# Kernel optimization log

Measured on AMD Instinct MI355X. Metric: run time of the kernel, lower is better.

Reference implementation:

```python
import jax, jax.numpy as jnp
import numpy as np

B, H, K, D = 4096, 512, 32, 20


def setup_inputs() -> dict:
    key = jax.random.key(0)
    k1, k2 = jax.random.split(key)
    hidden = jax.random.normal(k1, (B, H), dtype=jnp.float32)
    # cluster: soft assignment probabilities (rows sum to 1), like a softmax output
    c = jax.random.uniform(k2, (B, K), dtype=jnp.float32)
    cluster = c / jnp.sum(c, axis=-1, keepdims=True)
    return {"hidden": hidden, "cluster": cluster, "d": D}


def reference(hidden, cluster, d):
    # softHidden[b,h,k] = hidden[b,h] * cluster[b,k]
    soft_hidden = hidden[:, :, None] * cluster[:, None, :]          # [B,H,K]
    class_sums = jnp.sum(soft_hidden, axis=0)                        # [H,K] (code calls these "class_means" but they are sums)
    within = jnp.sum((soft_hidden - class_sums[None]) ** 2, axis=0)  # [H,K]
    # round() has zero gradient in torch; mirror that with stop_gradient
    counts = jax.lax.stop_gradient(jnp.round(jnp.sum(cluster, axis=0)))  # [K]

    m = class_sums.T   # [K,H]
    w = within.T       # [K,H]

    # all class pairs i<j (the nested Python loops, vectorized)
    i, j = jnp.triu_indices(K, k=1)   # each [P], P = K*(K-1)/2
    mi, mj = m[i], m[j]                               # [P,H]
    gm = (mi + mj) / 2.0
    between = (mi - gm) ** 2 * counts[i][:, None] + (mj - gm) ** 2 * counts[j][:, None]
    pair_within = w[i] + w[j]                         # [P,H]
    pair_count = counts[i] + counts[j]                # [P]

    d2 = pair_count - 2.0
    d2 = jnp.where(d2 == 0.0, d2 + 1e-5, d2)
    x = between / (between + pair_within)
    x = jnp.clip(x, 1e-37, 1.0 - 1e-5)
    # regularized incomplete beta I_x(d1/2, d2/2) with d1 = 1
    xbetainc = jax.scipy.special.betainc(0.5, (d2 / 2.0)[:, None], x)  # [P,H]

    top_k, _ = jax.lax.top_k(xbetainc, d)             # [P,d]
    per_pair = jnp.sum(jnp.log(top_k), axis=-1)       # [P]
    return -jnp.sum(per_pair)
```

## Files before the change

kernel.cpp:

```cpp
#include <hip/hip_runtime.h>
#include <math.h>

#define BB 4096
#define HH 512
#define KK 32
#define PAIRS ((KK * (KK - 1)) / 2)

constexpr int TH  = 16;
constexpr int NBB = 16;
constexpr int BC  = BB / NBB;
constexpr int SUB = 64;
constexpr int RP  = TH + 1;


__global__ __launch_bounds__(256) void stage1_kernel(
    const float* __restrict__ hidden, const float* __restrict__ cluster,
    float* __restrict__ part_m, float* __restrict__ part_s,
    float* __restrict__ pcol, float* __restrict__ ctl)
{
    __shared__ float hid_s[SUB * TH];
    __shared__ float clu_s[SUB * KK];
    __shared__ float red  [8 * KK * RP];
    __shared__ float cred [8 * KK];

    const int t  = threadIdx.x;
    const int ty = t >> 5;
    const int tx = t & 31;
    const int h0 = blockIdx.x * TH;
    const int c  = blockIdx.y;
    const int bchunk = c * BC;

    if (blockIdx.x == 0 && c == 0 && t == 0) {
        ctl[0] = 0.0f;
        ((unsigned*)ctl)[1] = 0u;
    }

    float acc_m[TH], acc_s[TH];
#pragma unroll
    for (int i = 0; i < TH; ++i) { acc_m[i] = 0.f; acc_s[i] = 0.f; }
    float csum = 0.f;

    const float4* hid4 = (const float4*)hidden;
    const float4* clu4 = (const float4*)cluster;

    for (int sub = 0; sub < BC; sub += SUB) {
        const int b0 = bchunk + sub;
        {
            int r = t >> 2, q = t & 3;
            ((float4*)hid_s)[t] =
                hid4[(size_t)(b0 + r) * (HH / 4) + (h0 >> 2) + q];
        }
#pragma unroll
        for (int e = 0; e < 2; ++e) {
            int u = t + e * 256;
            int r = u >> 3, q = u & 7;
            ((float4*)clu_s)[u] = clu4[(size_t)(b0 + r) * (KK / 4) + q];
        }
        __syncthreads();

#pragma unroll
        for (int s = 0; s < SUB / 8; ++s) {
            int r = s * 8 + ty;
            float cc = clu_s[r * KK + tx];
            float c2 = cc * cc;
            csum += cc;
#pragma unroll
            for (int hh = 0; hh < TH; ++hh) {
                float hv = hid_s[r * TH + hh];
                acc_m[hh] = fmaf(hv,      cc, acc_m[hh]);
                acc_s[hh] = fmaf(hv * hv, c2, acc_s[hh]);
            }
        }
        __syncthreads();
    }

    cred[ty * KK + tx] = csum;
    __syncthreads();
    if (blockIdx.x == 0 && t < KK) {
        float v = 0.f;
#pragma unroll
        for (int g = 0; g < 8; ++g) v += cred[g * KK + t];
        pcol[c * KK + t] = v;
    }

#pragma unroll
    for (int hh = 0; hh < TH; ++hh)
        red[ty * (KK * RP) + tx * RP + hh] = acc_m[hh];
    __syncthreads();
    for (int u = t; u < KK * TH; u += 256) {
        int k = u >> 4, hh = u & 15;
        float v = 0.f;
#pragma unroll
        for (int g = 0; g < 8; ++g) v += red[g * (KK * RP) + k * RP + hh];
        part_m[((size_t)c * KK + k) * HH + h0 + hh] = v;
    }
    __syncthreads();
#pragma unroll
    for (int hh = 0; hh < TH; ++hh)
        red[ty * (KK * RP) + tx * RP + hh] = acc_s[hh];
    __syncthreads();
    for (int u = t; u < KK * TH; u += 256) {
        int k = u >> 4, hh = u & 15;
        float v = 0.f;
#pragma unroll
        for (int g = 0; g < 8; ++g) v += red[g * (KK * RP) + k * RP + hh];
        part_s[((size_t)c * KK + k) * HH + h0 + hh] = v;
    }
}

__device__ __forceinline__ float frcp(float x) {
#if __has_builtin(__builtin_amdgcn_rcpf)
    return __builtin_amdgcn_rcpf(x);
#else
    return 1.0f / x;
#endif
}
__device__ __forceinline__ float guardf(float t) {
    return (fabsf(t) < 1e-30f) ? 1e-30f : t;
}

__device__ float betacf_fast(float a, float b, float x)
{
    const float EPS = 1e-5f;
    float qab = a + b, qap = a + 1.0f, qam = a - 1.0f;
    float c = 1.0f;
    float d = frcp(guardf(1.0f - qab * x * frcp(qap)));
    float h = d;
    for (int m = 1; m <= 100; ++m) {
        float fm = (float)m, m2 = 2.0f * fm;
        float aa = fm * (b - fm) * x * frcp((qam + m2) * (a + m2));
        d = frcp(guardf(fmaf(aa, d, 1.0f)));
        c = guardf(fmaf(aa, frcp(c), 1.0f));
        h *= d * c;
        float aa2 = -(a + fm) * (qab + fm) * x * frcp((a + m2) * (qap + m2));
        d = frcp(guardf(fmaf(aa2, d, 1.0f)));
        c = guardf(fmaf(aa2, frcp(c), 1.0f));
        float del = d * c;
        h *= del;
        if (__all(fabsf(del - 1.0f) < EPS)) break;
    }
    return h;
}

__global__ __launch_bounds__(256) void stage2_kernel(
    const float* __restrict__ part_m, const float* __restrict__ part_s,
    const float* __restrict__ pcol, float* __restrict__ ctl,
    const int* __restrict__ dptr, float* __restrict__ out)
{
    __shared__ float xs[HH];

    const int t = threadIdx.x;
    const int w = t >> 6, lane = t & 63;
    const int p = blockIdx.x;

    int i = 0, rem = p;
    while (true) { int row = KK - 1 - i; if (rem < row) break; rem -= row; ++i; }
    const int j = i + 1 + rem;

    float ci = 0.f, cj = 0.f;
#pragma unroll
    for (int cc = 0; cc < NBB; ++cc) {
        ci += pcol[cc * KK + i];
        cj += pcol[cc * KK + j];
    }
    ci = roundf(ci); cj = roundf(cj);
    const float pc = ci + cj;
    float d2 = pc - 2.0f;
    if (d2 == 0.0f) d2 = 1e-5f;
    const float a = 0.5f;
    const float b = 0.5f * d2;

#pragma unroll
    for (int q = 0; q < 2; ++q) {
        int h = w * 128 + q * 64 + lane;
        float mi = 0.f, mj = 0.f, si = 0.f, sj = 0.f;
#pragma unroll
        for (int cc = 0; cc < NBB; ++cc) {
            size_t base = (size_t)cc * KK * HH;
            mi += part_m[base + (size_t)i * HH + h];
            mj += part_m[base + (size_t)j * HH + h];
            si += part_s[base + (size_t)i * HH + h];
            sj += part_s[base + (size_t)j * HH + h];
        }
        float wi = fmaf((float)(BB - 2) * mi, mi, si);
        float wj = fmaf((float)(BB - 2) * mj, mj, sj);
        float dm = 0.5f * (mi - mj);
        float between = dm * dm * pc;
        float denom = between + wi + wj;
        float x = between / denom;
        if (!(x >= 1e-37f)) x = 1e-37f;
        x = fminf(x, 1.0f - 1e-5f);
        xs[h] = x;
    }
    __syncthreads();
    if (w != 0) return;

    float lv[8];
#pragma unroll
    for (int q = 0; q < 8; ++q) lv[q] = xs[q * 64 + lane];

    const int d = *dptr;
    const float lg = lgammaf(a + b) - lgammaf(b) - 0.57236494f;
    const float xsplit = (a + 1.0f) / (a + b + 2.0f);

    float myx = 0.004f;
    float lm = lv[0];
#pragma unroll
    for (int q = 1; q < 8; ++q) lm = fmaxf(lm, lv[q]);

    for (int r = 0; r < d; ++r) {
        float gm = lm;
#pragma unroll
        for (int off = 1; off < 64; off <<= 1)
            gm = fmaxf(gm, __shfl_xor(gm, off));
        unsigned long long msk = __ballot(lm == gm);
        int winner = __ffsll((unsigned long long)msk) - 1;
        if (lane == r) myx = gm;
        if (lane == winner) {
            bool done = false;
#pragma unroll
            for (int q = 0; q < 8; ++q)
                if (!done && lv[q] == gm) { lv[q] = -1.0f; done = true; }
            lm = lv[0];
#pragma unroll
            for (int q = 1; q < 8; ++q) lm = fmaxf(lm, lv[q]);
        }
    }

    float x   = myx;
    float omx = 1.0f - x;
    bool  brA = x < xsplit;
    float al  = brA ? a : b;
    float be  = brA ? b : a;
    float xx  = brA ? x : omx;
    float cf  = betacf_fast(al, be, xx);
    float lbt = lg + 0.5f * logf(x) + b * logf(omx);
    float L;
    if (brA) {
        L = lbt + logf(2.0f * fmaxf(cf, 1e-30f));
    } else {
        float tt = expf(lbt) * cf / b;
        tt = fminf(tt, 0.99999988f);
        L = log1pf(-tt);
    }

    float val = (lane < d) ? L : 0.0f;
#pragma unroll
    for (int off = 1; off < 64; off <<= 1) val += __shfl_xor(val, off);

    if (lane == 0) {
        atomicAdd(&ctl[0], -val);
        __threadfence();
        unsigned old = atomicAdd((unsigned*)ctl + 1, 1u);
        if (old == PAIRS - 1) {
            out[0] = atomicAdd(&ctl[0], 0.0f);
        }
    }
}

extern "C" void kernel_launch(void* const* d_in, const int* in_sizes, int n_in,
                              void* d_out, int out_size, void* d_ws, size_t ws_size,
                              hipStream_t stream)
{
    const float* hidden  = (const float*)d_in[0];
    const float* cluster = (const float*)d_in[1];
    const int*   dptr    = (const int*)d_in[2];

    float* part_m = (float*)d_ws;
    float* part_s = part_m + (size_t)NBB * KK * HH;
    float* pcol   = part_s + (size_t)NBB * KK * HH;
    float* ctl    = pcol + NBB * KK;

    dim3 g1(HH / TH, NBB);
    stage1_kernel<<<g1, 256, 0, stream>>>(hidden, cluster,
                                          part_m, part_s, pcol, ctl);
    stage2_kernel<<<PAIRS, 256, 0, stream>>>(part_m, part_s, pcol, ctl,
                                             dptr, (float*)d_out);
}
```

Measured before the change: 95.35 us.

## Replace continued-fraction betainc with closed-form series for integer degrees of freedom

For integer d2 (the Student-t style case with a=1/2), stage2 now evaluates the regularized incomplete beta with a finite closed-form series. The series uses compile-time coefficient tables plus asin for odd cases, and it replaces the iterative Lentz continued fraction and lgamma calls. Stage1 also precomputes squared hidden values into shared memory and reads hidden tiles as float4, which cuts per-element multiplies and LDS instructions. The series loop length grows with d2 (around 128 here), so the cost is a table-driven loop with global constant loads, and the old path remains as a fallback for non-integer values.

```diff
diff --git a/kernel.cpp b/kernel.cpp
--- a/kernel.cpp
+++ b/kernel.cpp
@@ -12,16 +12,33 @@
 constexpr int SUB = 64;
 constexpr int RP  = TH + 1;
 
+struct TabE {
+    float v[2048];
+    constexpr TabE() : v{} {
+        double c = 1.0; v[0] = 1.0f;
+        for (int j = 1; j < 2048; ++j) { c *= (2.0*j - 1.0) / (2.0*j); v[j] = (float)c; }
+    }
+};
+struct TabO {
+    float v[2048];
+    constexpr TabO() : v{} {
+        double c = 1.0; v[0] = 1.0f;
+        for (int j = 1; j < 2048; ++j) { c *= (2.0*j) / (2.0*j + 1.0); v[j] = (float)c; }
+    }
+};
+__device__ constexpr TabE tab_e{};
+__device__ constexpr TabO tab_o{};
 
 __global__ __launch_bounds__(256) void stage1_kernel(
     const float* __restrict__ hidden, const float* __restrict__ cluster,
     float* __restrict__ part_m, float* __restrict__ part_s,
     float* __restrict__ pcol, float* __restrict__ ctl)
 {
-    __shared__ float hid_s[SUB * TH];
-    __shared__ float clu_s[SUB * KK];
-    __shared__ float red  [8 * KK * RP];
-    __shared__ float cred [8 * KK];
+    __shared__ float hid_s [SUB * TH];
+    __shared__ float hid2_s[SUB * TH];
+    __shared__ float clu_s [SUB * KK];
+    __shared__ float red   [8 * KK * RP];
+    __shared__ float cred  [8 * KK];
 
     const int t  = threadIdx.x;
     const int ty = t >> 5;
@@ -47,8 +64,10 @@
         const int b0 = bchunk + sub;
         {
             int r = t >> 2, q = t & 3;
-            ((float4*)hid_s)[t] =
-                hid4[(size_t)(b0 + r) * (HH / 4) + (h0 >> 2) + q];
+            float4 v = hid4[(size_t)(b0 + r) * (HH / 4) + (h0 >> 2) + q];
+            ((float4*)hid_s)[t] = v;
+            float4 v2; v2.x = v.x*v.x; v2.y = v.y*v.y; v2.z = v.z*v.z; v2.w = v.w*v.w;
+            ((float4*)hid2_s)[t] = v2;
         }
 #pragma unroll
         for (int e = 0; e < 2; ++e) {
@@ -58,18 +77,32 @@
         }
         __syncthreads();
 
+        const float4* h4 = (const float4*)hid_s;
+        const float4* g4 = (const float4*)hid2_s;
 #pragma unroll
         for (int s = 0; s < SUB / 8; ++s) {
             int r = s * 8 + ty;
             float cc = clu_s[r * KK + tx];
             float c2 = cc * cc;
             csum += cc;
-#pragma unroll
-            for (int hh = 0; hh < TH; ++hh) {
-                float hv = hid_s[r * TH + hh];
-                acc_m[hh] = fmaf(hv,      cc, acc_m[hh]);
-                acc_s[hh] = fmaf(hv * hv, c2, acc_s[hh]);
-            }
+            float4 a0 = h4[r*4+0], a1 = h4[r*4+1], a2 = h4[r*4+2], a3 = h4[r*4+3];
+            float4 b0 = g4[r*4+0], b1 = g4[r*4+1], b2 = g4[r*4+2], b3 = g4[r*4+3];
+            acc_m[0]  = fmaf(a0.x, cc, acc_m[0]);  acc_m[1]  = fmaf(a0.y, cc, acc_m[1]);
+            acc_m[2]  = fmaf(a0.z, cc, acc_m[2]);  acc_m[3]  = fmaf(a0.w, cc, acc_m[3]);
+            acc_m[4]  = fmaf(a1.x, cc, acc_m[4]);  acc_m[5]  = fmaf(a1.y, cc, acc_m[5]);
+            acc_m[6]  = fmaf(a1.z, cc, acc_m[6]);  acc_m[7]  = fmaf(a1.w, cc, acc_m[7]);
+            acc_m[8]  = fmaf(a2.x, cc, acc_m[8]);  acc_m[9]  = fmaf(a2.y, cc, acc_m[9]);
+            acc_m[10] = fmaf(a2.z, cc, acc_m[10]); acc_m[11] = fmaf(a2.w, cc, acc_m[11]);
+            acc_m[12] = fmaf(a3.x, cc, acc_m[12]); acc_m[13] = fmaf(a3.y, cc, acc_m[13]);
+            acc_m[14] = fmaf(a3.z, cc, acc_m[14]); acc_m[15] = fmaf(a3.w, cc, acc_m[15]);
+            acc_s[0]  = fmaf(b0.x, c2, acc_s[0]);  acc_s[1]  = fmaf(b0.y, c2, acc_s[1]);
+            acc_s[2]  = fmaf(b0.z, c2, acc_s[2]);  acc_s[3]  = fmaf(b0.w, c2, acc_s[3]);
+            acc_s[4]  = fmaf(b1.x, c2, acc_s[4]);  acc_s[5]  = fmaf(b1.y, c2, acc_s[5]);
+            acc_s[6]  = fmaf(b1.z, c2, acc_s[6]);  acc_s[7]  = fmaf(b1.w, c2, acc_s[7]);
+            acc_s[8]  = fmaf(b2.x, c2, acc_s[8]);  acc_s[9]  = fmaf(b2.y, c2, acc_s[9]);
+            acc_s[10] = fmaf(b2.z, c2, acc_s[10]); acc_s[11] = fmaf(b2.w, c2, acc_s[11]);
+            acc_s[12] = fmaf(b3.x, c2, acc_s[12]); acc_s[13] = fmaf(b3.y, c2, acc_s[13]);
+            acc_s[14] = fmaf(b3.z, c2, acc_s[14]); acc_s[15] = fmaf(b3.w, c2, acc_s[15]);
         }
         __syncthreads();
     }
@@ -167,7 +200,6 @@
     const float pc = ci + cj;
     float d2 = pc - 2.0f;
     if (d2 == 0.0f) d2 = 1e-5f;
-    const float a = 0.5f;
     const float b = 0.5f * d2;
 
 #pragma unroll
@@ -200,9 +232,6 @@
     for (int q = 0; q < 8; ++q) lv[q] = xs[q * 64 + lane];
 
     const int d = *dptr;
-    const float lg = lgammaf(a + b) - lgammaf(b) - 0.57236494f;
-    const float xsplit = (a + 1.0f) / (a + b + 2.0f);
-
     float myx = 0.004f;
     float lm = lv[0];
 #pragma unroll
@@ -227,21 +256,60 @@
         }
     }
 
-    float x   = myx;
-    float omx = 1.0f - x;
-    bool  brA = x < xsplit;
-    float al  = brA ? a : b;
-    float be  = brA ? b : a;
-    float xx  = brA ? x : omx;
-    float cf  = betacf_fast(al, be, xx);
-    float lbt = lg + 0.5f * logf(x) + b * logf(omx);
+    float x  = myx;
+    float u  = 1.0f - x;
+    float sx = sqrtf(x);
+    int nu = (int)(d2 + 0.5f);
     float L;
-    if (brA) {
-        L = lbt + logf(2.0f * fmaxf(cf, 1e-30f));
+    if (nu >= 1 && nu <= 4094 && fabsf(d2 - (float)nu) < 1e-3f) {
+        float u2 = u * u;
+        if (nu & 1) {
+            int terms = (nu - 1) >> 1;
+            float S = 0.f;
+            if (terms > 0) {
+                float S0 = 0.f, S1 = 0.f, p0 = 1.f, p1 = u;
+                int jj = 0;
+                for (; jj + 1 < terms; jj += 2) {
+                    S0 = fmaf(tab_o.v[jj],     p0, S0);
+                    S1 = fmaf(tab_o.v[jj + 1], p1, S1);
+                    p0 *= u2; p1 *= u2;
+                }
+                if (jj < terms) S0 = fmaf(tab_o.v[jj], p0, S0);
+                S = S0 + S1;
+            }
+            float theta = asinf(fminf(sx, 1.0f));
+            float A = 0.636619772367581343f * (theta + sx * sqrtf(u) * S);
+            L = logf(fminf(A, 1.0f));
+        } else {
+            int terms = nu >> 1;
+            float S0 = 0.f, S1 = 0.f, p0 = 1.f, p1 = u;
+            int jj = 0;
+            for (; jj + 1 < terms; jj += 2) {
+                S0 = fmaf(tab_e.v[jj],     p0, S0);
+                S1 = fmaf(tab_e.v[jj + 1], p1, S1);
+                p0 *= u2; p1 *= u2;
+            }
+            if (jj < terms) S0 = fmaf(tab_e.v[jj], p0, S0);
+            float A = sx * (S0 + S1);
+            L = logf(fminf(A, 1.0f));
+        }
     } else {
-        float tt = expf(lbt) * cf / b;
-        tt = fminf(tt, 0.99999988f);
-        L = log1pf(-tt);
+        const float a = 0.5f;
+        const float lg = lgammaf(a + b) - lgammaf(b) - 0.57236494f;
+        const float xsplit = (a + 1.0f) / (a + b + 2.0f);
+        bool  brA = x < xsplit;
+        float al  = brA ? a : b;
+        float be  = brA ? b : a;
+        float xx  = brA ? x : u;
+        float cf  = betacf_fast(al, be, xx);
+        float lbt = lg + 0.5f * logf(x) + b * logf(u);
+        if (brA) {
+            L = lbt + logf(2.0f * fmaxf(cf, 1e-30f));
+        } else {
+            float tt = expf(lbt) * cf / b;
+            tt = fminf(tt, 0.99999988f);
+            L = log1pf(-tt);
+        }
     }
 
     float val = (lane < d) ? L : 0.0f;
```

Result: no change. 96.30 us (+1.0%).
